# Performance work log

Hardware: AMD Instinct MI355X
Metric: run time of the kernel (lower is better)

The kernel has to match this reference:

```python
import jax, jax.numpy as jnp
import numpy as np

B, T, D = 4, 2048, 768
H = 12
DH = D // H  # 64
SCALE = DH ** -0.5


def setup_inputs() -> dict:
    key = jax.random.key(0)
    k1, k2, k3, k4 = jax.random.split(key, 4)
    x = jax.random.normal(k1, (B, T, D), dtype=jnp.float32)
    # torch nn.Linear weights: stored [out, in], applied as x @ W.T
    Wqkv = jax.random.normal(k2, (3 * D, D), dtype=jnp.float32) * (D ** -0.5)
    Wproj = jax.random.normal(k3, (D, D), dtype=jnp.float32) * (D ** -0.5)
    bproj = jax.random.normal(k4, (D,), dtype=jnp.float32) * 0.01
    return {"x": x, "Wqkv": Wqkv, "Wproj": Wproj, "bproj": bproj}


def reference(x, Wqkv, Wproj, bproj):
    Bb, Tt, C = x.shape
    qkv = x @ Wqkv.T                       # [B,T,3D]
    q, k, v = jnp.split(qkv, 3, axis=-1)   # each [B,T,D]
    q = q.reshape(Bb, Tt, H, DH)
    k = k.reshape(Bb, Tt, H, DH)
    v = v.reshape(Bb, Tt, H, DH)
    # scores [B,H,T,T]
    att = jnp.einsum('bqhd,bkhd->bhqk', q, k) * SCALE
    causal = jnp.triu(jnp.ones((Tt, Tt), dtype=bool), k=1)
    att = jnp.where(causal, -jnp.inf, att)
    att = jax.nn.softmax(att, axis=-1)
    out = jnp.einsum('bhqk,bkhd->bqhd', att, v).reshape(Bb, Tt, C)
    return out @ Wproj.T + bproj
```

## Files before the change

kernel.cpp:

```cpp
#include <hip/hip_runtime.h>
#include <hip/hip_bf16.h>


#define BATCH  4
#define SEQ    2048
#define DMODEL 768
#define NH     12
#define DHEAD  64
static constexpr float SCALE_LOG2E = 0.125f * 1.4426950408889634f;

#define N_X  (8192 * 768)
#define N_WQ (2304 * 768)
#define N_WP (768 * 768)

typedef __bf16 v8bf __attribute__((ext_vector_type(8)));
typedef float  v4f  __attribute__((ext_vector_type(4)));

__device__ __forceinline__ v8bf cvt8(const float* __restrict__ p) {
    const float4 a = ((const float4*)p)[0];
    const float4 b = ((const float4*)p)[1];
    v8bf r;
    r[0] = (__bf16)a.x; r[1] = (__bf16)a.y; r[2] = (__bf16)a.z; r[3] = (__bf16)a.w;
    r[4] = (__bf16)b.x; r[5] = (__bf16)b.y; r[6] = (__bf16)b.z; r[7] = (__bf16)b.w;
    return r;
}

__device__ __forceinline__ void async_copy16(__bf16* lds, const __bf16* g) {
    __builtin_amdgcn_global_load_lds(
        (const __attribute__((address_space(1))) void*)g,
        (__attribute__((address_space(3))) void*)lds, 16, 0, 0);
}

__global__ __launch_bounds__(256) void cvt_kernel(
        const float* __restrict__ x, const float* __restrict__ Wq,
        const float* __restrict__ Wp, __bf16* __restrict__ xb,
        __bf16* __restrict__ Wqb, __bf16* __restrict__ Wpb) {
    const long e = ((long)blockIdx.x * 256 + threadIdx.x) * 8;
    const float* src;
    __bf16* dst;
    if (e < N_X)             { src = x  + e;               dst = xb  + e; }
    else if (e < N_X + N_WQ) { src = Wq + (e - N_X);        dst = Wqb + (e - N_X); }
    else                     { src = Wp + (e - N_X - N_WQ); dst = Wpb + (e - N_X - N_WQ); }
    *(v8bf*)dst = cvt8(src);
}

__global__ __launch_bounds__(256) void qkv_gemm(
        const __bf16* __restrict__ xb, const __bf16* __restrict__ Wb,
        __bf16* __restrict__ Qb, __bf16* __restrict__ Kb, __bf16* __restrict__ Vtb) {
    __shared__ __bf16 As[128 * 32], Bs[128 * 32];
    const int lane = threadIdx.x & 63, wave = threadIdx.x >> 6;
    const int nb = blockIdx.x % 18, mb = blockIdx.x / 18;
    const int r16 = lane & 15, quad = lane >> 4;
    const int wm = (wave >> 1) * 64, wn = (wave & 1) * 64;
    const __bf16* Asrc = xb + (size_t)mb * 128 * DMODEL;
    const __bf16* Bsrc = Wb + (size_t)nb * 128 * DMODEL;

    v4f acc[4][4] = {};
    for (int k0 = 0; k0 < DMODEL; k0 += 32) {
#pragma unroll
        for (int p = 0; p < 2; ++p) {
            const int cb = p * 256 + wave * 64;
            const int c = cb + lane;
            const int row = c >> 2, sg = c & 3;
            async_copy16(&As[cb * 8], Asrc + (size_t)row * DMODEL + k0 + sg * 8);
            async_copy16(&Bs[cb * 8], Bsrc + (size_t)row * DMODEL + k0 + sg * 8);
        }
        __syncthreads();
        v8bf a[4], b[4];
#pragma unroll
        for (int i = 0; i < 4; ++i)
            a[i] = *(const v8bf*)&As[(wm + 16 * i + r16) * 32 + quad * 8];
#pragma unroll
        for (int j = 0; j < 4; ++j)
            b[j] = *(const v8bf*)&Bs[(wn + 16 * j + r16) * 32 + quad * 8];
#pragma unroll
        for (int i = 0; i < 4; ++i)
#pragma unroll
            for (int j = 0; j < 4; ++j)
                acc[i][j] = __builtin_amdgcn_mfma_f32_16x16x32_bf16(
                    a[i], b[j], acc[i][j], 0, 0, 0);
        __syncthreads();
    }

    const int seg = nb / 6;
    const int nl0 = (nb % 6) * 128 + wn;
#pragma unroll
    for (int j = 0; j < 4; ++j) {
        const int n = nl0 + 16 * j + r16;
        const int h = n >> 6, d = n & 63;
#pragma unroll
        for (int i = 0; i < 4; ++i) {
            const int mrow = mb * 128 + wm + 16 * i + quad * 4;
#pragma unroll
            for (int r = 0; r < 4; ++r) {
                const int m = mrow + r;
                const int bidx = m >> 11, t = m & (SEQ - 1);
                const size_t base = ((size_t)(bidx * NH + h)) * SEQ * DHEAD;
                if (seg == 0)
                    Qb[base + (size_t)t * DHEAD + d] = (__bf16)(acc[i][j][r] * SCALE_LOG2E);
                else if (seg == 1)
                    Kb[base + (size_t)t * DHEAD + d] = (__bf16)acc[i][j][r];
                else
                    Vtb[base + (size_t)d * SEQ + t] = (__bf16)acc[i][j][r];
            }
        }
    }
}

__global__ __launch_bounds__(256, 3) void attn_kernel(
        const __bf16* __restrict__ Qb, const __bf16* __restrict__ Kb,
        const __bf16* __restrict__ Vtb, __bf16* __restrict__ attnb) {
    __shared__ __bf16 Ks[2][64 * 32];
    __shared__ __bf16 Vs[2][64 * 32];
    __shared__ __align__(16) __bf16 Pl[4][32 * 72];
    const int lane = threadIdx.x & 63;
    const int wave = threadIdx.x >> 6;
    const int bh = blockIdx.x % 48;
    const int qt = 15 - (blockIdx.x / 48);
    const int q0 = qt * 128 + wave * 32;
    const int r16 = lane & 15, quad = lane >> 4;

    const __bf16* Q  = Qb  + (size_t)bh * SEQ * DHEAD;
    const __bf16* K  = Kb  + (size_t)bh * SEQ * DHEAD;
    const __bf16* Vt = Vtb + (size_t)bh * DHEAD * SEQ;

    const int srow  = wave * 16 + (lane >> 2);
    const int skoff = (lane & 3) * 8;
    __bf16* kd0 = &Ks[0][wave * 512];
    __bf16* kd1 = &Ks[1][wave * 512];
    __bf16* vd0 = &Vs[0][wave * 512];
    __bf16* vd1 = &Vs[1][wave * 512];

    v8bf aq[2][2];
#pragma unroll
    for (int i = 0; i < 2; ++i)
#pragma unroll
        for (int kk = 0; kk < 2; ++kk)
            aq[i][kk] = *(const v8bf*)(Q + (size_t)(q0 + 16 * i + r16) * DHEAD
                                         + kk * 32 + quad * 8);

    v8bf vones;
#pragma unroll
    for (int j = 0; j < 8; ++j) vones[j] = (__bf16)1.0f;

    v4f oacc[2][4] = {};
    v4f lacc[2] = {};

    const int nchunks = 2 * (qt + 1);
    async_copy16(kd0, K + (size_t)srow * DHEAD + skoff);
    async_copy16(kd1, K + (size_t)srow * DHEAD + 32 + skoff);
    async_copy16(vd0, Vt + (size_t)srow * SEQ + skoff);
    async_copy16(vd1, Vt + (size_t)srow * SEQ + 32 + skoff);

    for (int c = 0; c < nchunks; ++c) {
        const int k0 = c * 64;
        __syncthreads();
        v8bf bk[4][2], bv[2][4];
#pragma unroll
        for (int s = 0; s < 4; ++s)
#pragma unroll
            for (int kk = 0; kk < 2; ++kk)
                bk[s][kk] = *(const v8bf*)&Ks[kk][(16 * s + r16) * 32 + quad * 8];
#pragma unroll
        for (int kk = 0; kk < 2; ++kk)
#pragma unroll
            for (int n = 0; n < 4; ++n)
                bv[kk][n] = *(const v8bf*)&Vs[kk][(16 * n + r16) * 32 + quad * 8];
        __syncthreads();
        if (c + 1 < nchunks) {
            const int k1 = k0 + 64;
            async_copy16(kd0, K + (size_t)(k1 / 64 * 64 + srow) * DHEAD + skoff);
            async_copy16(kd1, K + (size_t)(k1 / 64 * 64 + srow) * DHEAD + 32 + skoff);
            async_copy16(vd0, Vt + (size_t)srow * SEQ + k1 + skoff);
            async_copy16(vd1, Vt + (size_t)srow * SEQ + k1 + 32 + skoff);
        }
        if (k0 > q0 + 31) continue;

        v4f sc[2][4] = {};
#pragma unroll
        for (int kk = 0; kk < 2; ++kk)
#pragma unroll
            for (int i = 0; i < 2; ++i)
#pragma unroll
                for (int s = 0; s < 4; ++s)
                    sc[i][s] = __builtin_amdgcn_mfma_f32_16x16x32_bf16(
                        aq[i][kk], bk[s][kk], sc[i][s], 0, 0, 0);

        if (k0 + 63 > q0) {
#pragma unroll
            for (int i = 0; i < 2; ++i)
#pragma unroll
                for (int s = 0; s < 4; ++s)
#pragma unroll
                    for (int r = 0; r < 4; ++r) {
                        const int row = q0 + 16 * i + quad * 4 + r;
                        const int col = k0 + 16 * s + r16;
                        if (col > row) sc[i][s][r] = -1e30f;
                    }
        }

#pragma unroll
        for (int i = 0; i < 2; ++i)
#pragma unroll
            for (int s = 0; s < 4; ++s)
#pragma unroll
                for (int r = 0; r < 4; ++r)
                    sc[i][s][r] = __builtin_exp2f(sc[i][s][r] - 32.0f);

#pragma unroll
        for (int i = 0; i < 2; ++i)
#pragma unroll
            for (int s = 0; s < 4; ++s)
#pragma unroll
                for (int r = 0; r < 4; ++r)
                    Pl[wave][(16 * i + quad * 4 + r) * 72 + 16 * s + r16] =
                        (__bf16)sc[i][s][r];
        __builtin_amdgcn_s_waitcnt(0);

        v8bf ap[2][2];
#pragma unroll
        for (int i = 0; i < 2; ++i)
#pragma unroll
            for (int kk = 0; kk < 2; ++kk)
                ap[i][kk] = *(const v8bf*)&Pl[wave][(16 * i + r16) * 72 + kk * 32 + quad * 8];
#pragma unroll
        for (int kk = 0; kk < 2; ++kk)
#pragma unroll
            for (int i = 0; i < 2; ++i) {
#pragma unroll
                for (int n = 0; n < 4; ++n)
                    oacc[i][n] = __builtin_amdgcn_mfma_f32_16x16x32_bf16(
                        ap[i][kk], bv[kk][n], oacc[i][n], 0, 0, 0);
                lacc[i] = __builtin_amdgcn_mfma_f32_16x16x32_bf16(
                    ap[i][kk], vones, lacc[i], 0, 0, 0);
            }
    }

    const int b = bh / NH, h = bh - b * NH;
#pragma unroll
    for (int i = 0; i < 2; ++i)
#pragma unroll
        for (int r = 0; r < 4; ++r) {
            const float inv = 1.0f / lacc[i][r];
            const int t = q0 + 16 * i + quad * 4 + r;
#pragma unroll
            for (int n = 0; n < 4; ++n) {
                const int d = 16 * n + r16;
                attnb[((size_t)(b * SEQ + t)) * DMODEL + h * DHEAD + d] =
                    (__bf16)(oacc[i][n][r] * inv);
            }
        }
}

__global__ __launch_bounds__(256) void proj_gemm(
        const __bf16* __restrict__ Ab, const __bf16* __restrict__ Wb,
        const float* __restrict__ bias, float* __restrict__ out) {
    __shared__ __bf16 As[128 * 32], Bs[128 * 32];
    const int lane = threadIdx.x & 63, wave = threadIdx.x >> 6;
    const int nb = blockIdx.x % 6, mb = blockIdx.x / 6;
    const int r16 = lane & 15, quad = lane >> 4;
    const int wm = (wave >> 1) * 64, wn = (wave & 1) * 64;
    const __bf16* Asrc = Ab + (size_t)mb * 128 * DMODEL;
    const __bf16* Bsrc = Wb + (size_t)nb * 128 * DMODEL;

    v4f acc[4][4] = {};
    for (int k0 = 0; k0 < DMODEL; k0 += 32) {
#pragma unroll
        for (int p = 0; p < 2; ++p) {
            const int cb = p * 256 + wave * 64;
            const int c = cb + lane;
            const int row = c >> 2, sg = c & 3;
            async_copy16(&As[cb * 8], Asrc + (size_t)row * DMODEL + k0 + sg * 8);
            async_copy16(&Bs[cb * 8], Bsrc + (size_t)row * DMODEL + k0 + sg * 8);
        }
        __syncthreads();
        v8bf a[4], b[4];
#pragma unroll
        for (int i = 0; i < 4; ++i)
            a[i] = *(const v8bf*)&As[(wm + 16 * i + r16) * 32 + quad * 8];
#pragma unroll
        for (int j = 0; j < 4; ++j)
            b[j] = *(const v8bf*)&Bs[(wn + 16 * j + r16) * 32 + quad * 8];
#pragma unroll
        for (int i = 0; i < 4; ++i)
#pragma unroll
            for (int j = 0; j < 4; ++j)
                acc[i][j] = __builtin_amdgcn_mfma_f32_16x16x32_bf16(
                    a[i], b[j], acc[i][j], 0, 0, 0);
        __syncthreads();
    }

#pragma unroll
    for (int j = 0; j < 4; ++j) {
        const int n = nb * 128 + wn + 16 * j + r16;
        const float bv = bias[n];
#pragma unroll
        for (int i = 0; i < 4; ++i) {
            const int mrow = mb * 128 + wm + 16 * i + quad * 4;
#pragma unroll
            for (int r = 0; r < 4; ++r)
                out[(size_t)(mrow + r) * DMODEL + n] = acc[i][j][r] + bv;
        }
    }
}

extern "C" void kernel_launch(void* const* d_in, const int* in_sizes, int n_in,
                              void* d_out, int out_size, void* d_ws, size_t ws_size,
                              hipStream_t stream) {
    const float* x     = (const float*)d_in[0];
    const float* Wqkv  = (const float*)d_in[1];
    const float* Wproj = (const float*)d_in[2];
    const float* bproj = (const float*)d_in[3];
    float* out = (float*)d_out;

    char* ws = (char*)d_ws;
    const size_t tsz = (size_t)BATCH * NH * SEQ * DHEAD * sizeof(__bf16);
    __bf16* Qb    = (__bf16*)(ws);
    __bf16* Kb    = (__bf16*)(ws + tsz);
    __bf16* Vtb   = (__bf16*)(ws + 2 * tsz);
    __bf16* xb    = (__bf16*)(ws + 3 * tsz);
    __bf16* attnb = (__bf16*)(ws + 3 * tsz);
    __bf16* Wqb   = (__bf16*)(ws + 4 * tsz);
    __bf16* Wpb   = (__bf16*)(ws + 4 * tsz + (size_t)N_WQ * 2);

    cvt_kernel<<<dim3((N_X + N_WQ + N_WP) / (8 * 256)), dim3(256), 0, stream>>>(
        x, Wqkv, Wproj, xb, Wqb, Wpb);
    qkv_gemm<<<dim3(64 * 18), dim3(256), 0, stream>>>(xb, Wqb, Qb, Kb, Vtb);
    attn_kernel<<<dim3(16 * 48), dim3(256), 0, stream>>>(Qb, Kb, Vtb, attnb);
    proj_gemm<<<dim3(64 * 6), dim3(256), 0, stream>>>(attnb, Wpb, bproj, out);
}
```

Measured before the change: 239.6 us.

## Double-buffer and XOR-swizzle LDS tiles in QKV and projection GEMMs

Both GEMM kernels now keep two LDS buffers for the A and B tiles. The next k-slice's async copies are issued before the current slice's MFMAs, and the trailing barrier is removed, so global loads can overlap compute. The LDS layout is XOR-swizzled on the 16-byte segment index to reduce bank conflicts on fragment reads. This doubles the shared memory per block, which may lower occupancy. A redundant index expression in the attention K prefetch is also simplified.

```diff
diff --git a/kernel.cpp b/kernel.cpp
--- a/kernel.cpp
+++ b/kernel.cpp
@@ -47,7 +47,7 @@
 __global__ __launch_bounds__(256) void qkv_gemm(
         const __bf16* __restrict__ xb, const __bf16* __restrict__ Wb,
         __bf16* __restrict__ Qb, __bf16* __restrict__ Kb, __bf16* __restrict__ Vtb) {
-    __shared__ __bf16 As[128 * 32], Bs[128 * 32];
+    __shared__ __bf16 As[2][128 * 32], Bs[2][128 * 32];
     const int lane = threadIdx.x & 63, wave = threadIdx.x >> 6;
     const int nb = blockIdx.x % 18, mb = blockIdx.x / 18;
     const int r16 = lane & 15, quad = lane >> 4;
@@ -55,31 +55,45 @@
     const __bf16* Asrc = xb + (size_t)mb * 128 * DMODEL;
     const __bf16* Bsrc = Wb + (size_t)nb * 128 * DMODEL;
 
+    const int srow = wave * 16 + (lane >> 2);
+    const int sg   = lane & 3;
+    const int g    = sg ^ ((srow >> 1) & 3);
+    const size_t soff0 = (size_t)srow * DMODEL + g * 8;
+    const size_t soff1 = (size_t)(srow + 64) * DMODEL + g * 8;
+    const int ld0 = wave * 512;
+    const int ld1 = 2048 + wave * 512;
+    const int p_rd = quad ^ ((r16 >> 1) & 3);
+
+    async_copy16(&As[0][ld0], Asrc + soff0);
+    async_copy16(&As[0][ld1], Asrc + soff1);
+    async_copy16(&Bs[0][ld0], Bsrc + soff0);
+    async_copy16(&Bs[0][ld1], Bsrc + soff1);
+
     v4f acc[4][4] = {};
-    for (int k0 = 0; k0 < DMODEL; k0 += 32) {
-#pragma unroll
-        for (int p = 0; p < 2; ++p) {
-            const int cb = p * 256 + wave * 64;
-            const int c = cb + lane;
-            const int row = c >> 2, sg = c & 3;
-            async_copy16(&As[cb * 8], Asrc + (size_t)row * DMODEL + k0 + sg * 8);
-            async_copy16(&Bs[cb * 8], Bsrc + (size_t)row * DMODEL + k0 + sg * 8);
-        }
+    for (int c = 0; c < 24; ++c) {
+        const int cur = c & 1;
         __syncthreads();
         v8bf a[4], b[4];
 #pragma unroll
         for (int i = 0; i < 4; ++i)
-            a[i] = *(const v8bf*)&As[(wm + 16 * i + r16) * 32 + quad * 8];
+            a[i] = *(const v8bf*)&As[cur][(wm + 16 * i + r16) * 32 + p_rd * 8];
 #pragma unroll
         for (int j = 0; j < 4; ++j)
-            b[j] = *(const v8bf*)&Bs[(wn + 16 * j + r16) * 32 + quad * 8];
+            b[j] = *(const v8bf*)&Bs[cur][(wn + 16 * j + r16) * 32 + p_rd * 8];
+        if (c + 1 < 24) {
+            const int nxt = cur ^ 1;
+            const size_t k1 = (c + 1) * 32;
+            async_copy16(&As[nxt][ld0], Asrc + soff0 + k1);
+            async_copy16(&As[nxt][ld1], Asrc + soff1 + k1);
+            async_copy16(&Bs[nxt][ld0], Bsrc + soff0 + k1);
+            async_copy16(&Bs[nxt][ld1], Bsrc + soff1 + k1);
+        }
 #pragma unroll
         for (int i = 0; i < 4; ++i)
 #pragma unroll
             for (int j = 0; j < 4; ++j)
                 acc[i][j] = __builtin_amdgcn_mfma_f32_16x16x32_bf16(
                     a[i], b[j], acc[i][j], 0, 0, 0);
-        __syncthreads();
     }
 
     const int seg = nb / 6;
@@ -169,8 +183,8 @@
         __syncthreads();
         if (c + 1 < nchunks) {
             const int k1 = k0 + 64;
-            async_copy16(kd0, K + (size_t)(k1 / 64 * 64 + srow) * DHEAD + skoff);
-            async_copy16(kd1, K + (size_t)(k1 / 64 * 64 + srow) * DHEAD + 32 + skoff);
+            async_copy16(kd0, K + (size_t)(k1 + srow) * DHEAD + skoff);
+            async_copy16(kd1, K + (size_t)(k1 + srow) * DHEAD + 32 + skoff);
             async_copy16(vd0, Vt + (size_t)srow * SEQ + k1 + skoff);
             async_copy16(vd1, Vt + (size_t)srow * SEQ + k1 + 32 + skoff);
         }
@@ -255,7 +269,7 @@
 __global__ __launch_bounds__(256) void proj_gemm(
         const __bf16* __restrict__ Ab, const __bf16* __restrict__ Wb,
         const float* __restrict__ bias, float* __restrict__ out) {
-    __shared__ __bf16 As[128 * 32], Bs[128 * 32];
+    __shared__ __bf16 As[2][128 * 32], Bs[2][128 * 32];
     const int lane = threadIdx.x & 63, wave = threadIdx.x >> 6;
     const int nb = blockIdx.x % 6, mb = blockIdx.x / 6;
     const int r16 = lane & 15, quad = lane >> 4;
@@ -263,31 +277,45 @@
     const __bf16* Asrc = Ab + (size_t)mb * 128 * DMODEL;
     const __bf16* Bsrc = Wb + (size_t)nb * 128 * DMODEL;
 
+    const int srow = wave * 16 + (lane >> 2);
+    const int sg   = lane & 3;
+    const int g    = sg ^ ((srow >> 1) & 3);
+    const size_t soff0 = (size_t)srow * DMODEL + g * 8;
+    const size_t soff1 = (size_t)(srow + 64) * DMODEL + g * 8;
+    const int ld0 = wave * 512;
+    const int ld1 = 2048 + wave * 512;
+    const int p_rd = quad ^ ((r16 >> 1) & 3);
+
+    async_copy16(&As[0][ld0], Asrc + soff0);
+    async_copy16(&As[0][ld1], Asrc + soff1);
+    async_copy16(&Bs[0][ld0], Bsrc + soff0);
+    async_copy16(&Bs[0][ld1], Bsrc + soff1);
+
     v4f acc[4][4] = {};
-    for (int k0 = 0; k0 < DMODEL; k0 += 32) {
-#pragma unroll
-        for (int p = 0; p < 2; ++p) {
-            const int cb = p * 256 + wave * 64;
-            const int c = cb + lane;
-            const int row = c >> 2, sg = c & 3;
-            async_copy16(&As[cb * 8], Asrc + (size_t)row * DMODEL + k0 + sg * 8);
-            async_copy16(&Bs[cb * 8], Bsrc + (size_t)row * DMODEL + k0 + sg * 8);
-        }
+    for (int c = 0; c < 24; ++c) {
+        const int cur = c & 1;
         __syncthreads();
         v8bf a[4], b[4];
 #pragma unroll
         for (int i = 0; i < 4; ++i)
-            a[i] = *(const v8bf*)&As[(wm + 16 * i + r16) * 32 + quad * 8];
+            a[i] = *(const v8bf*)&As[cur][(wm + 16 * i + r16) * 32 + p_rd * 8];
 #pragma unroll
         for (int j = 0; j < 4; ++j)
-            b[j] = *(const v8bf*)&Bs[(wn + 16 * j + r16) * 32 + quad * 8];
+            b[j] = *(const v8bf*)&Bs[cur][(wn + 16 * j + r16) * 32 + p_rd * 8];
+        if (c + 1 < 24) {
+            const int nxt = cur ^ 1;
+            const size_t k1 = (c + 1) * 32;
+            async_copy16(&As[nxt][ld0], Asrc + soff0 + k1);
+            async_copy16(&As[nxt][ld1], Asrc + soff1 + k1);
+            async_copy16(&Bs[nxt][ld0], Bsrc + soff0 + k1);
+            async_copy16(&Bs[nxt][ld1], Bsrc + soff1 + k1);
+        }
 #pragma unroll
         for (int i = 0; i < 4; ++i)
 #pragma unroll
             for (int j = 0; j < 4; ++j)
                 acc[i][j] = __builtin_amdgcn_mfma_f32_16x16x32_bf16(
                     a[i], b[j], acc[i][j], 0, 0, 0);
-        __syncthreads();
     }
 
 #pragma unroll
```

Measured after the change: 233.4 us. 1.03x faster.

## Restructure GEMMs to stage full-K weight panel in LDS and stream A from global

Applied to the files above, without the earlier changes.

Both QKV and projection GEMMs now load an entire 48-row weight panel (all of K) into swizzled LDS once, then each wave streams its 32 A rows directly from global memory with no per-K-step barriers. Tiles shrink from 128x128 to 128x48, so the grid is larger and the per-iteration syncs are gone. The V-transpose store is vectorised to 4-wide bf16. Smaller tiles lower MFMA reuse per A load, LDS use per block rises to about 72KB, and A reads now go through global/cache, not LDS.

```diff
diff --git a/kernel.cpp b/kernel.cpp
--- a/kernel.cpp
+++ b/kernel.cpp
@@ -14,6 +14,7 @@
 #define N_WP (768 * 768)
 
 typedef __bf16 v8bf __attribute__((ext_vector_type(8)));
+typedef __bf16 v4bf __attribute__((ext_vector_type(4)));
 typedef float  v4f  __attribute__((ext_vector_type(4)));
 
 __device__ __forceinline__ v8bf cvt8(const float* __restrict__ p) {
@@ -44,64 +45,83 @@
     *(v8bf*)dst = cvt8(src);
 }
 
+__device__ __forceinline__ void stage_bpanel(__bf16* Bl, const __bf16* Bsrc,
+                                             int wave, int lane) {
+#pragma unroll
+    for (int a = 0; a < 18; ++a) {
+        const int ub = a * 256 + wave * 64;
+        const int u = ub + lane;
+        const int row = u / 96;
+        const int kgl = u - row * 96;
+        const int kgs = kgl ^ (row & 7);
+        async_copy16(Bl + (size_t)ub * 8,
+                     Bsrc + (size_t)row * DMODEL + kgs * 8);
+    }
+}
+
 __global__ __launch_bounds__(256) void qkv_gemm(
         const __bf16* __restrict__ xb, const __bf16* __restrict__ Wb,
         __bf16* __restrict__ Qb, __bf16* __restrict__ Kb, __bf16* __restrict__ Vtb) {
-    __shared__ __bf16 As[128 * 32], Bs[128 * 32];
+    __shared__ __bf16 Bl[48 * DMODEL];
     const int lane = threadIdx.x & 63, wave = threadIdx.x >> 6;
-    const int nb = blockIdx.x % 18, mb = blockIdx.x / 18;
+    const int p  = blockIdx.x >> 6;
+    const int mb = blockIdx.x & 63;
     const int r16 = lane & 15, quad = lane >> 4;
-    const int wm = (wave >> 1) * 64, wn = (wave & 1) * 64;
     const __bf16* Asrc = xb + (size_t)mb * 128 * DMODEL;
-    const __bf16* Bsrc = Wb + (size_t)nb * 128 * DMODEL;
-
-    v4f acc[4][4] = {};
-    for (int k0 = 0; k0 < DMODEL; k0 += 32) {
-#pragma unroll
-        for (int p = 0; p < 2; ++p) {
-            const int cb = p * 256 + wave * 64;
-            const int c = cb + lane;
-            const int row = c >> 2, sg = c & 3;
-            async_copy16(&As[cb * 8], Asrc + (size_t)row * DMODEL + k0 + sg * 8);
-            async_copy16(&Bs[cb * 8], Bsrc + (size_t)row * DMODEL + k0 + sg * 8);
-        }
-        __syncthreads();
-        v8bf a[4], b[4];
-#pragma unroll
-        for (int i = 0; i < 4; ++i)
-            a[i] = *(const v8bf*)&As[(wm + 16 * i + r16) * 32 + quad * 8];
-#pragma unroll
-        for (int j = 0; j < 4; ++j)
-            b[j] = *(const v8bf*)&Bs[(wn + 16 * j + r16) * 32 + quad * 8];
-#pragma unroll
-        for (int i = 0; i < 4; ++i)
-#pragma unroll
-            for (int j = 0; j < 4; ++j)
+    const __bf16* Bsrc = Wb + (size_t)p * 48 * DMODEL;
+
+    stage_bpanel(Bl, Bsrc, wave, lane);
+    __syncthreads();
+
+    const int m0 = wave * 32;
+    const int sw = r16 & 7;
+    v4f acc[2][3] = {};
+#pragma unroll 4
+    for (int c = 0; c < 24; ++c) {
+        v8bf af[2], bf_[3];
+#pragma unroll
+        for (int i = 0; i < 2; ++i)
+            af[i] = *(const v8bf*)(Asrc + (size_t)(m0 + 16 * i + r16) * DMODEL
+                                        + c * 32 + quad * 8);
+#pragma unroll
+        for (int j = 0; j < 3; ++j) {
+            const int row = 16 * j + r16;
+            const int kg = (4 * c + quad) ^ sw;
+            bf_[j] = *(const v8bf*)&Bl[((size_t)row * 96 + kg) * 8];
+        }
+#pragma unroll
+        for (int i = 0; i < 2; ++i)
+#pragma unroll
+            for (int j = 0; j < 3; ++j)
                 acc[i][j] = __builtin_amdgcn_mfma_f32_16x16x32_bf16(
-                    a[i], b[j], acc[i][j], 0, 0, 0);
-        __syncthreads();
-    }
-
-    const int seg = nb / 6;
-    const int nl0 = (nb % 6) * 128 + wn;
-#pragma unroll
-    for (int j = 0; j < 4; ++j) {
-        const int n = nl0 + 16 * j + r16;
+                    af[i], bf_[j], acc[i][j], 0, 0, 0);
+    }
+
+    const int seg = p >> 4;
+    const int nn0 = (p & 15) * 48;
+#pragma unroll
+    for (int j = 0; j < 3; ++j) {
+        const int n = nn0 + 16 * j + r16;
         const int h = n >> 6, d = n & 63;
 #pragma unroll
-        for (int i = 0; i < 4; ++i) {
-            const int mrow = mb * 128 + wm + 16 * i + quad * 4;
-#pragma unroll
-            for (int r = 0; r < 4; ++r) {
-                const int m = mrow + r;
-                const int bidx = m >> 11, t = m & (SEQ - 1);
-                const size_t base = ((size_t)(bidx * NH + h)) * SEQ * DHEAD;
-                if (seg == 0)
-                    Qb[base + (size_t)t * DHEAD + d] = (__bf16)(acc[i][j][r] * SCALE_LOG2E);
-                else if (seg == 1)
-                    Kb[base + (size_t)t * DHEAD + d] = (__bf16)acc[i][j][r];
-                else
-                    Vtb[base + (size_t)d * SEQ + t] = (__bf16)acc[i][j][r];
+        for (int i = 0; i < 2; ++i) {
+            const int mrow = mb * 128 + m0 + 16 * i + quad * 4;
+            const int bidx = mrow >> 11, t0 = mrow & (SEQ - 1);
+            const size_t base = ((size_t)(bidx * NH + h)) * SEQ * DHEAD;
+            if (seg == 2) {
+                v4bf pk;
+#pragma unroll
+                for (int r = 0; r < 4; ++r) pk[r] = (__bf16)acc[i][j][r];
+                *(v4bf*)&Vtb[base + (size_t)d * SEQ + t0] = pk;
+            } else if (seg == 0) {
+#pragma unroll
+                for (int r = 0; r < 4; ++r)
+                    Qb[base + (size_t)(t0 + r) * DHEAD + d] =
+                        (__bf16)(acc[i][j][r] * SCALE_LOG2E);
+            } else {
+#pragma unroll
+                for (int r = 0; r < 4; ++r)
+                    Kb[base + (size_t)(t0 + r) * DHEAD + d] = (__bf16)acc[i][j][r];
             }
         }
     }
@@ -169,8 +189,8 @@
         __syncthreads();
         if (c + 1 < nchunks) {
             const int k1 = k0 + 64;
-            async_copy16(kd0, K + (size_t)(k1 / 64 * 64 + srow) * DHEAD + skoff);
-            async_copy16(kd1, K + (size_t)(k1 / 64 * 64 + srow) * DHEAD + 32 + skoff);
+            async_copy16(kd0, K + (size_t)(k1 + srow) * DHEAD + skoff);
+            async_copy16(kd1, K + (size_t)(k1 + srow) * DHEAD + 32 + skoff);
             async_copy16(vd0, Vt + (size_t)srow * SEQ + k1 + skoff);
             async_copy16(vd1, Vt + (size_t)srow * SEQ + k1 + 32 + skoff);
         }
@@ -255,48 +275,48 @@
 __global__ __launch_bounds__(256) void proj_gemm(
         const __bf16* __restrict__ Ab, const __bf16* __restrict__ Wb,
         const float* __restrict__ bias, float* __restrict__ out) {
-    __shared__ __bf16 As[128 * 32], Bs[128 * 32];
+    __shared__ __bf16 Bl[48 * DMODEL];
     const int lane = threadIdx.x & 63, wave = threadIdx.x >> 6;
-    const int nb = blockIdx.x % 6, mb = blockIdx.x / 6;
+    const int p  = blockIdx.x >> 6;
+    const int mb = blockIdx.x & 63;
     const int r16 = lane & 15, quad = lane >> 4;
-    const int wm = (wave >> 1) * 64, wn = (wave & 1) * 64;
     const __bf16* Asrc = Ab + (size_t)mb * 128 * DMODEL;
-    const __bf16* Bsrc = Wb + (size_t)nb * 128 * DMODEL;
-
-    v4f acc[4][4] = {};
-    for (int k0 = 0; k0 < DMODEL; k0 += 32) {
-#pragma unroll
-        for (int p = 0; p < 2; ++p) {
-            const int cb = p * 256 + wave * 64;
-            const int c = cb + lane;
-            const int row = c >> 2, sg = c & 3;
-            async_copy16(&As[cb * 8], Asrc + (size_t)row * DMODEL + k0 + sg * 8);
-            async_copy16(&Bs[cb * 8], Bsrc + (size_t)row * DMODEL + k0 + sg * 8);
-        }
-        __syncthreads();
-        v8bf a[4], b[4];
-#pragma unroll
-        for (int i = 0; i < 4; ++i)
-            a[i] = *(const v8bf*)&As[(wm + 16 * i + r16) * 32 + quad * 8];
-#pragma unroll
-        for (int j = 0; j < 4; ++j)
-            b[j] = *(const v8bf*)&Bs[(wn + 16 * j + r16) * 32 + quad * 8];
-#pragma unroll
-        for (int i = 0; i < 4; ++i)
-#pragma unroll
-            for (int j = 0; j < 4; ++j)
+    const __bf16* Bsrc = Wb + (size_t)p * 48 * DMODEL;
+
+    stage_bpanel(Bl, Bsrc, wave, lane);
+    __syncthreads();
+
+    const int m0 = wave * 32;
+    const int sw = r16 & 7;
+    v4f acc[2][3] = {};
+#pragma unroll 4
+    for (int c = 0; c < 24; ++c) {
+        v8bf af[2], bf_[3];
+#pragma unroll
+        for (int i = 0; i < 2; ++i)
+            af[i] = *(const v8bf*)(Asrc + (size_t)(m0 + 16 * i + r16) * DMODEL
+                                        + c * 32 + quad * 8);
+#pragma unroll
+        for (int j = 0; j < 3; ++j) {
+            const int row = 16 * j + r16;
+            const int kg = (4 * c + quad) ^ sw;
+            bf_[j] = *(const v8bf*)&Bl[((size_t)row * 96 + kg) * 8];
+        }
+#pragma unroll
+        for (int i = 0; i < 2; ++i)
+#pragma unroll
+            for (int j = 0; j < 3; ++j)
                 acc[i][j] = __builtin_amdgcn_mfma_f32_16x16x32_bf16(
-                    a[i], b[j], acc[i][j], 0, 0, 0);
-        __syncthreads();
-    }
-
-#pragma unroll
-    for (int j = 0; j < 4; ++j) {
-        const int n = nb * 128 + wn + 16 * j + r16;
+                    af[i], bf_[j], acc[i][j], 0, 0, 0);
+    }
+
+#pragma unroll
+    for (int j = 0; j < 3; ++j) {
+        const int n = p * 48 + 16 * j + r16;
         const float bv = bias[n];
 #pragma unroll
-        for (int i = 0; i < 4; ++i) {
-            const int mrow = mb * 128 + wm + 16 * i + quad * 4;
+        for (int i = 0; i < 2; ++i) {
+            const int mrow = mb * 128 + m0 + 16 * i + quad * 4;
 #pragma unroll
             for (int r = 0; r < 4; ++r)
                 out[(size_t)(mrow + r) * DMODEL + n] = acc[i][j][r] + bv;
@@ -325,7 +345,7 @@
 
     cvt_kernel<<<dim3((N_X + N_WQ + N_WP) / (8 * 256)), dim3(256), 0, stream>>>(
         x, Wqkv, Wproj, xb, Wqb, Wpb);
-    qkv_gemm<<<dim3(64 * 18), dim3(256), 0, stream>>>(xb, Wqb, Qb, Kb, Vtb);
+    qkv_gemm<<<dim3(48 * 64), dim3(256), 0, stream>>>(xb, Wqb, Qb, Kb, Vtb);
     attn_kernel<<<dim3(16 * 48), dim3(256), 0, stream>>>(Qb, Kb, Vtb, attnb);
-    proj_gemm<<<dim3(64 * 6), dim3(256), 0, stream>>>(attnb, Wpb, bproj, out);
-}
+    proj_gemm<<<dim3(16 * 64), dim3(256), 0, stream>>>(attnb, Wpb, bproj, out);
+}
```

Result: slower. 254.7 us (+6.3%).
